# Optimization experiments

Measured on AMD Instinct MI355X. Metric: run time of the kernel, lower is better.

Reference implementation:

```python
import jax, jax.numpy as jnp
from jax import lax
import numpy as np

B = 64
INPUT_DIM = 500000
WIN = 500
N_WIN = INPUT_DIM // WIN  # 1000
HID = 30
ANC = 7
KS = 75
EPS = 1e-5


def setup_inputs() -> dict:
    key = jax.random.key(0)
    ks = jax.random.split(key, 8)
    x = jax.random.uniform(ks[0], (B, INPUT_DIM, 2), dtype=jnp.float32)
    # stacked per-window MLP params (PyTorch Linear default init scale ~ 1/sqrt(fan_in))
    W1 = jax.random.normal(ks[1], (N_WIN, WIN, HID), dtype=jnp.float32) / np.sqrt(WIN)
    b1 = jax.random.normal(ks[2], (N_WIN, HID), dtype=jnp.float32) * 0.01
    W2 = jax.random.normal(ks[3], (N_WIN, HID, ANC), dtype=jnp.float32) / np.sqrt(HID)
    b2 = jax.random.normal(ks[4], (N_WIN, ANC), dtype=jnp.float32) * 0.01
    conv_w = jax.random.normal(ks[5], (ANC, ANC, KS, 2), dtype=jnp.float32) / np.sqrt(ANC * KS * 2)
    conv_b = jax.random.normal(ks[6], (ANC,), dtype=jnp.float32) * 0.01
    return {"x": x, "W1": W1, "b1": b1, "W2": W2, "b2": b2,
            "conv_w": conv_w, "conv_b": conv_b}


def _forward_base(xw, W1, b1, W2, b2):
    h = jnp.einsum('bnwc,nwh->bnhc', xw, W1) + b1[None, :, :, None]
    h = jax.nn.relu(h)
    # BatchNorm1d (training mode, affine=False): batch stats per (window, hidden)
    # and per haplotype channel (the torch module is called once per haplotype).
    mean = jnp.mean(h, axis=0, keepdims=True)
    var = jnp.var(h, axis=0, keepdims=True)  # biased, matches torch BN normalization
    h = (h - mean) * lax.rsqrt(var + EPS)
    o = jnp.einsum('bnhc,nha->bnac', h, W2) + b2[None, :, :, None]  # [B,nW,A,2]
    return jnp.transpose(o, (0, 2, 1, 3))  # [B, A, nW, 2]


def reference(x, W1, b1, W2, b2, conv_w, conv_b):
    x = (x - 0.5) * 2.0
    xw = x[:, :N_WIN * WIN].reshape(B, N_WIN, WIN, 2)
    out_base = _forward_base(xw, W1, b1, W2, b2)  # [B, A, nW, 2]
    # smoother: softmax over ancestry dim, reflect-padded Conv2d
    p = jax.nn.softmax(out_base, axis=1)
    pad_h = KS // 2  # 37
    pp = jnp.pad(p, ((0, 0), (0, 0), (pad_h, pad_h), (1, 1)), mode='reflect')
    out = lax.conv_general_dilated(pp, conv_w, window_strides=(1, 1), padding='VALID',
                                   dimension_numbers=('NCHW', 'OIHW', 'NCHW'))
    out = out + conv_b[None, :, None, None]
    out_smooth = out[:, :, :, 0:2]  # crop to 2 haplotype columns
    return out_base, out_smooth
```

## Files before the change

kernel.cpp:

```cpp
#include <hip/hip_runtime.h>

#define NWIN 1000
#define WIN  500
#define HID  30
#define ANC  7
#define BATCH 64
#define KS   75
#define PADH 37
#define OBASE_ELEMS (BATCH*ANC*NWIN*2)

#define CK_W   25
#define NCK    20

#define XS(buf,c,b,q) ((((buf)*2+(c))*64+(b))*28 + (q))
#define WSO(buf,w,j)  (7168 + (buf)*800 + (w)*32 + (j))
#define HS(wh,b,col)  (((wh)*64+(b))*61 + (col))

__device__ __forceinline__ void gload_lds16(const float* g, float* l) {
    __builtin_amdgcn_global_load_lds(
        (const __attribute__((address_space(1))) void*)g,
        (__attribute__((address_space(3))) void*)l, 16, 0, 0);
}

__global__ __launch_bounds__(256, 4) void k1(
        const float* __restrict__ x,
        const float* __restrict__ W1, const float* __restrict__ b1,
        const float* __restrict__ W2, const float* __restrict__ b2,
        float* __restrict__ out_base)
{
    __shared__ float smem[8768];

    const int n    = blockIdx.x;
    const int t    = threadIdx.x;
    const int wid  = __builtin_amdgcn_readfirstlane(t >> 6);
    const int lane = t & 63;
    const int wh   = wid & 1;
    const int bh   = wid >> 1;
    const int bloc = lane & 31;
    const int cc   = lane >> 5;
    const int b    = bh * 32 + bloc;
    const int wh12 = wh * 12;

    float acc[30];
#pragma unroll
    for (int j = 0; j < 30; ++j) acc[j] = 0.f;

    float2 xr[7];

    const float2* __restrict__ x2 = reinterpret_cast<const float2*>(x);

    auto issue_x = [&](int ck) {
        const size_t base = (size_t)n * 500 + (size_t)ck * 25;
#pragma unroll
        for (int r = 0; r < 6; ++r) {
            const int g  = t + r * 256;
            const int bb = g / 25, q = g - bb * 25;
            xr[r] = x2[(size_t)bb * 500000 + base + q];
        }
        if (t < 64) {
            const int g  = t + 1536;
            const int bb = g / 25, q = g - bb * 25;
            xr[6] = x2[(size_t)bb * 500000 + base + q];
        }
    };

    auto commit_x = [&](int buf) {
#pragma unroll
        for (int r = 0; r < 6; ++r) {
            const int g  = t + r * 256;
            const int bb = g / 25, q = g - bb * 25;
            smem[XS(buf, 0, bb, q)] = xr[r].x;
            smem[XS(buf, 1, bb, q)] = xr[r].y;
        }
        if (t < 64) {
            const int g  = t + 1536;
            const int bb = g / 25, q = g - bb * 25;
            smem[XS(buf, 0, bb, q)] = xr[6].x;
            smem[XS(buf, 1, bb, q)] = xr[6].y;
        }
    };

    auto issue_w = [&](int ck, int buf) {
        if (t < 200) {
            const int w  = t >> 3, kq = t & 7;
            size_t off = (size_t)n * 15000 + (size_t)ck * 750 + w * 30 + kq * 4;
            if (off > 14999996u) off = 14999996u;
            gload_lds16(W1 + off, &smem[7168 + buf * 800 + (t & 192) * 4]);
        }
    };

    auto dot30 = [&](float xcomp, const float4* __restrict__ wrow) {
        const float xv = fmaf(2.f, xcomp, -1.f);
        float4 w8[8];
#pragma unroll
        for (int u = 0; u < 8; ++u) w8[u] = wrow[u];
#pragma unroll
        for (int j = 0; j < 30; ++j) {
            const float wv = ((const float*)&w8[j >> 2])[j & 3];
            acc[j] = fmaf(xv, wv, acc[j]);
        }
    };

    issue_w(0, 0);
    issue_x(0);
    commit_x(0);
    __syncthreads();

    for (int ck = 0; ck < NCK; ++ck) {
        const int cur = ck & 1, nxt = cur ^ 1;
        const bool pre = (ck < NCK - 1);
        if (pre) {
            issue_w(ck + 1, nxt);
            issue_x(ck + 1);
            __builtin_amdgcn_sched_barrier(0);
        }

        const float* __restrict__ xrow = &smem[XS(cur, cc, b, wh12)];
        const float4* __restrict__ wp  =
            reinterpret_cast<const float4*>(&smem[WSO(cur, wh12, 0)]);
        const float4* __restrict__ xr4 = reinterpret_cast<const float4*>(xrow);

#pragma unroll
        for (int g = 0; g < 3; ++g) {
            const float4 xq = xr4[g];
            dot30(xq.x, wp + (g * 4 + 0) * 8);
            dot30(xq.y, wp + (g * 4 + 1) * 8);
            dot30(xq.z, wp + (g * 4 + 2) * 8);
            dot30(xq.w, wp + (g * 4 + 3) * 8);
        }
        if (wh12) dot30(xrow[12], wp + 96);

        if (pre) commit_x(nxt);
        __syncthreads();
    }

#pragma unroll
    for (int j = 0; j < 30; ++j)
        smem[HS(wh, b, cc * 30 + j)] = acc[j];
    __syncthreads();

    {
        const int bb = t & 63;
        const int q2 = t >> 6;
        const int ch = q2 >> 1;
        const int jh = (q2 & 1) * 15;
        const float* __restrict__ b1p = b1 + n * HID + jh;
#pragma unroll
        for (int jj = 0; jj < 15; ++jj) {
            const int col = ch * 30 + jh + jj;
            float v = smem[HS(0, bb, col)] + smem[HS(1, bb, col)] + b1p[jj];
            v = fmaxf(v, 0.f);
            float s = v, ss = v * v;
#pragma unroll
            for (int off = 32; off > 0; off >>= 1) {
                s  += __shfl_xor(s, off);
                ss += __shfl_xor(ss, off);
            }
            const float mean = s * (1.f / 64.f);
            const float var  = ss * (1.f / 64.f) - mean * mean;
            const float rn   = rsqrtf(var + 1e-5f);
            smem[HS(0, bb, col)] = (v - mean) * rn;
        }
    }
    __syncthreads();

    const float* __restrict__ w2p = W2 + (size_t)n * (HID * ANC);
    float2* __restrict__ ob2 = reinterpret_cast<float2*>(out_base);
    for (int idx = t; idx < BATCH * ANC; idx += 256) {
        const int bb = idx / 7, a = idx - bb * 7;
        float o0 = b2[n * ANC + a], o1 = o0;
#pragma unroll
        for (int h = 0; h < HID; ++h) {
            const float wv = w2p[h * ANC + a];
            o0 = fmaf(smem[HS(0, bb, h)],      wv, o0);
            o1 = fmaf(smem[HS(0, bb, 30 + h)], wv, o1);
        }
        ob2[((size_t)bb * ANC + a) * NWIN + n] = make_float2(o0, o1);
    }
}

__global__ __launch_bounds__(256, 2) void k2(
        const float* __restrict__ out_base,
        const float* __restrict__ conv_w, const float* __restrict__ conv_b,
        float* __restrict__ out_smooth)
{
    __shared__ float2 sdl[199 * ANC];
    __shared__ float2 wael[ANC * ANC * KS];

    const int bidx = blockIdx.x;
    const int b  = bidx >> 3;
    const int ht = bidx & 7;
    const int h0 = ht * 125;
    const int t  = threadIdx.x;

    const float2* __restrict__ cw2 = reinterpret_cast<const float2*>(conv_w);
    for (int idx = t; idx < ANC * ANC * KS; idx += 256) {
        const float2 w = cw2[idx];
        wael[idx] = make_float2(w.x + w.y, w.x - w.y);
    }

    if (t < 199) {
        const int hglob = h0 - PADH + t;
        const int hm = hglob < 0 ? -hglob
                     : (hglob >= NWIN ? 2 * NWIN - 2 - hglob : hglob);
        float p[2][ANC];
#pragma unroll
        for (int c = 0; c < 2; ++c) {
            float v[ANC];
            float m = -1e30f;
#pragma unroll
            for (int a = 0; a < ANC; ++a) {
                v[a] = out_base[(((size_t)b * ANC + a) * NWIN + hm) * 2 + c];
                m = fmaxf(m, v[a]);
            }
            float s = 0.f;
#pragma unroll
            for (int a = 0; a < ANC; ++a) { v[a] = __expf(v[a] - m); s += v[a]; }
            const float inv = 1.f / s;
#pragma unroll
            for (int a = 0; a < ANC; ++a) p[c][a] = v[a] * inv;
        }
#pragma unroll
        for (int a = 0; a < ANC; ++a)
            sdl[t * ANC + a] = make_float2(p[0][a] + p[1][a], p[0][a] - p[1][a]);
    }
    __syncthreads();

    for (int idx = t; idx < ANC * 125; idx += 256) {
        const int o  = idx / 125;
        const int hl = idx % 125;
        float sa = 0.f, de = 0.f;
        const float2* __restrict__ wrow = &wael[o * ANC * KS];
#pragma unroll 1
        for (int i = 0; i < ANC; ++i) {
            const float2* __restrict__ sdp = &sdl[hl * ANC + i];
            const float2* __restrict__ wp  = &wrow[i * KS];
#pragma unroll 5
            for (int kh = 0; kh < KS; ++kh) {
                const float2 sd = sdp[kh * ANC];
                const float2 we = wp[kh];
                sa = fmaf(sd.x, we.x, sa);
                de = fmaf(sd.y, we.y, de);
            }
        }
        const float cb = conv_b[o];
        const float o0 = 0.5f * (sa - de) + cb;
        const float o1 = 0.5f * (sa + de) + cb;
        const size_t base = (((size_t)b * ANC + o) * NWIN + (h0 + hl)) * 2;
        out_smooth[base + 0] = o0;
        out_smooth[base + 1] = o1;
    }
}

extern "C" void kernel_launch(void* const* d_in, const int* in_sizes, int n_in,
                              void* d_out, int out_size, void* d_ws, size_t ws_size,
                              hipStream_t stream)
{
    const float* x      = (const float*)d_in[0];
    const float* W1     = (const float*)d_in[1];
    const float* b1     = (const float*)d_in[2];
    const float* W2     = (const float*)d_in[3];
    const float* b2     = (const float*)d_in[4];
    const float* conv_w = (const float*)d_in[5];
    const float* conv_b = (const float*)d_in[6];
    float* out = (float*)d_out;

    k1<<<dim3(NWIN), dim3(256), 0, stream>>>(x, W1, b1, W2, b2, out);
    k2<<<dim3(BATCH * 8), dim3(256), 0, stream>>>(out, conv_w, conv_b,
                                                  out + OBASE_ELEMS);
}
```

Baseline: 202.9 us.

## Register-tile first-layer GEMM as 4x8x2 outer products with wave-split reduction

Restructures the per-window first-layer matmul. Each lane now computes a 4-batch by 8-hidden by 2-channel register tile using float4 LDS loads of x and W1, in place of one batch row against all 30 hidden units. The 500-element window is split into 24-element chunks, and each of the four waves handles 6 positions. Partial sums are reduced across waves through shared memory in two phases. The x affine transform and zero padding past the window end are applied when staging x into LDS. The aim is to cut LDS traffic per FMA and to drop the per-FMA x rescale, at the cost of one extra chunk iteration, some wasted hidden columns (32 vs 30), and an extra reduction barrier.

```diff
diff --git a/kernel.cpp b/kernel.cpp
--- a/kernel.cpp
+++ b/kernel.cpp
@@ -9,12 +9,12 @@
 #define PADH 37
 #define OBASE_ELEMS (BATCH*ANC*NWIN*2)
 
-#define CK_W   25
-#define NCK    20
-
-#define XS(buf,c,b,q) ((((buf)*2+(c))*64+(b))*28 + (q))
-#define WSO(buf,w,j)  (7168 + (buf)*800 + (w)*32 + (j))
-#define HS(wh,b,col)  (((wh)*64+(b))*61 + (col))
+#define CK   24
+#define NCK  21
+
+#define XB(buf,c,p,b) ((buf)*3264 + ((c)*24+(p))*68 + (b))
+#define WB(buf,p,j)   (6528 + (buf)*768 + (p)*32 + (j))
+#define HS(ph,b,col)  (((ph)*64+(b))*61 + (col))
 
 __device__ __forceinline__ void gload_lds16(const float* g, float* l) {
     __builtin_amdgcn_global_load_lds(
@@ -28,82 +28,68 @@
         const float* __restrict__ W2, const float* __restrict__ b2,
         float* __restrict__ out_base)
 {
-    __shared__ float smem[8768];
+    __shared__ float smem[8064];
 
     const int n    = blockIdx.x;
     const int t    = threadIdx.x;
     const int wid  = __builtin_amdgcn_readfirstlane(t >> 6);
     const int lane = t & 63;
-    const int wh   = wid & 1;
-    const int bh   = wid >> 1;
-    const int bloc = lane & 31;
-    const int cc   = lane >> 5;
-    const int b    = bh * 32 + bloc;
-    const int wh12 = wh * 12;
-
-    float acc[30];
-#pragma unroll
-    for (int j = 0; j < 30; ++j) acc[j] = 0.f;
-
-    float2 xr[7];
+    const int bq   = lane & 15;
+    const int jq   = lane >> 4;
+    const int b0   = bq * 4;
+    const int j0   = jq * 8;
+
+    float acc[4][8][2];
+#pragma unroll
+    for (int i = 0; i < 4; ++i)
+#pragma unroll
+        for (int j = 0; j < 8; ++j) { acc[i][j][0] = 0.f; acc[i][j][1] = 0.f; }
+
+    int sb[6], sp[6];
+#pragma unroll
+    for (int r = 0; r < 6; ++r) {
+        const int idx = t + r * 256;
+        sb[r] = idx / 24;
+        sp[r] = idx % 24;
+    }
 
     const float2* __restrict__ x2 = reinterpret_cast<const float2*>(x);
+    float2 xr[6];
 
     auto issue_x = [&](int ck) {
-        const size_t base = (size_t)n * 500 + (size_t)ck * 25;
 #pragma unroll
         for (int r = 0; r < 6; ++r) {
-            const int g  = t + r * 256;
-            const int bb = g / 25, q = g - bb * 25;
-            xr[r] = x2[(size_t)bb * 500000 + base + q];
-        }
-        if (t < 64) {
-            const int g  = t + 1536;
-            const int bb = g / 25, q = g - bb * 25;
-            xr[6] = x2[(size_t)bb * 500000 + base + q];
+            size_t flat = (size_t)sb[r] * 500000u + (size_t)n * 500u
+                        + (size_t)ck * CK + sp[r];
+            if (flat > 31999999u) flat = 31999999u;
+            xr[r] = x2[flat];
         }
     };
 
-    auto commit_x = [&](int buf) {
+    auto commit_x = [&](int buf, int ck) {
 #pragma unroll
         for (int r = 0; r < 6; ++r) {
-            const int g  = t + r * 256;
-            const int bb = g / 25, q = g - bb * 25;
-            smem[XS(buf, 0, bb, q)] = xr[r].x;
-            smem[XS(buf, 1, bb, q)] = xr[r].y;
-        }
-        if (t < 64) {
-            const int g  = t + 1536;
-            const int bb = g / 25, q = g - bb * 25;
-            smem[XS(buf, 0, bb, q)] = xr[6].x;
-            smem[XS(buf, 1, bb, q)] = xr[6].y;
+            const int gp = ck * CK + sp[r];
+            const bool ok = gp < 500;
+            const float f0 = ok ? fmaf(2.f, xr[r].x, -1.f) : 0.f;
+            const float f1 = ok ? fmaf(2.f, xr[r].y, -1.f) : 0.f;
+            smem[XB(buf, 0, sp[r], sb[r])] = f0;
+            smem[XB(buf, 1, sp[r], sb[r])] = f1;
         }
     };
 
     auto issue_w = [&](int ck, int buf) {
-        if (t < 200) {
-            const int w  = t >> 3, kq = t & 7;
-            size_t off = (size_t)n * 15000 + (size_t)ck * 750 + w * 30 + kq * 4;
+        if (t < 192) {
+            size_t off = (size_t)n * 15000u + (size_t)(ck * CK + (t >> 3)) * 30u
+                       + (size_t)(t & 7) * 4u;
             if (off > 14999996u) off = 14999996u;
-            gload_lds16(W1 + off, &smem[7168 + buf * 800 + (t & 192) * 4]);
-        }
-    };
-
-    auto dot30 = [&](float xcomp, const float4* __restrict__ wrow) {
-        const float xv = fmaf(2.f, xcomp, -1.f);
-        float4 w8[8];
-#pragma unroll
-        for (int u = 0; u < 8; ++u) w8[u] = wrow[u];
-#pragma unroll
-        for (int j = 0; j < 30; ++j) {
-            const float wv = ((const float*)&w8[j >> 2])[j & 3];
-            acc[j] = fmaf(xv, wv, acc[j]);
+            gload_lds16(W1 + off, &smem[WB(buf, 0, 0) + (t & 192) * 4]);
         }
     };
 
     issue_w(0, 0);
     issue_x(0);
-    commit_x(0);
+    commit_x(0, 0);
     __syncthreads();
 
     for (int ck = 0; ck < NCK; ++ck) {
@@ -115,28 +101,55 @@
             __builtin_amdgcn_sched_barrier(0);
         }
 
-        const float* __restrict__ xrow = &smem[XS(cur, cc, b, wh12)];
-        const float4* __restrict__ wp  =
-            reinterpret_cast<const float4*>(&smem[WSO(cur, wh12, 0)]);
-        const float4* __restrict__ xr4 = reinterpret_cast<const float4*>(xrow);
-
-#pragma unroll
-        for (int g = 0; g < 3; ++g) {
-            const float4 xq = xr4[g];
-            dot30(xq.x, wp + (g * 4 + 0) * 8);
-            dot30(xq.y, wp + (g * 4 + 1) * 8);
-            dot30(xq.z, wp + (g * 4 + 2) * 8);
-            dot30(xq.w, wp + (g * 4 + 3) * 8);
-        }
-        if (wh12) dot30(xrow[12], wp + 96);
-
-        if (pre) commit_x(nxt);
+        const int pb = wid * 6;
+#pragma unroll
+        for (int i = 0; i < 6; ++i) {
+            const int p = pb + i;
+            const float4 xa = *reinterpret_cast<const float4*>(&smem[XB(cur, 0, p, b0)]);
+            const float4 xb = *reinterpret_cast<const float4*>(&smem[XB(cur, 1, p, b0)]);
+            const float4 w0 = *reinterpret_cast<const float4*>(&smem[WB(cur, p, j0)]);
+            const float4 w1 = *reinterpret_cast<const float4*>(&smem[WB(cur, p, j0 + 4)]);
+            const float xav[4] = {xa.x, xa.y, xa.z, xa.w};
+            const float xbv[4] = {xb.x, xb.y, xb.z, xb.w};
+            const float wv[8]  = {w0.x, w0.y, w0.z, w0.w, w1.x, w1.y, w1.z, w1.w};
+#pragma unroll
+            for (int ii = 0; ii < 4; ++ii)
+#pragma unroll
+                for (int jj = 0; jj < 8; ++jj) {
+                    acc[ii][jj][0] = fmaf(xav[ii], wv[jj], acc[ii][jj][0]);
+                    acc[ii][jj][1] = fmaf(xbv[ii], wv[jj], acc[ii][jj][1]);
+                }
+        }
+
+        if (pre) commit_x(nxt, ck + 1);
         __syncthreads();
     }
 
-#pragma unroll
-    for (int j = 0; j < 30; ++j)
-        smem[HS(wh, b, cc * 30 + j)] = acc[j];
+    if (wid < 2) {
+#pragma unroll
+        for (int ii = 0; ii < 4; ++ii)
+#pragma unroll
+            for (int jj = 0; jj < 8; ++jj) {
+                const int j = j0 + jj;
+                if (j < 30) {
+                    smem[HS(wid, b0 + ii, j)]      = acc[ii][jj][0];
+                    smem[HS(wid, b0 + ii, 30 + j)] = acc[ii][jj][1];
+                }
+            }
+    }
+    __syncthreads();
+    if (wid >= 2) {
+#pragma unroll
+        for (int ii = 0; ii < 4; ++ii)
+#pragma unroll
+            for (int jj = 0; jj < 8; ++jj) {
+                const int j = j0 + jj;
+                if (j < 30) {
+                    smem[HS(wid - 2, b0 + ii, j)]      += acc[ii][jj][0];
+                    smem[HS(wid - 2, b0 + ii, 30 + j)] += acc[ii][jj][1];
+                }
+            }
+    }
     __syncthreads();
 
     {
```

After: 293.5 us. 44.6% more time.
